# Kernel tuning notes

Measured on AMD Instinct MI355X. Metric: run time of the kernel, lower is better.

Reference implementation:

```python
import jax, jax.numpy as jnp
import numpy as np

B, T, V = 8, 2048, 4096
BEAM = 8      # beam_size
BLANK = 0     # blank_id=0 in CTCBeamDecoder
TMP = 1.0     # temperature self.tmp


def setup_inputs() -> dict:
    key = jax.random.key(0)
    k1, k2 = jax.random.split(key)
    logits = jax.random.normal(k1, (B, T, V), dtype=jnp.float32)
    # valid frame counts in [T//2, T]
    lengths = jax.random.randint(k2, (B,), T // 2, T + 1).astype(jnp.int32)
    return {"logits": logits, "lengths": lengths}


def _beam_search_single(logP, length):
    """CTC beam search over alignments (no LM) for one utterance.
    logP: [T, V] log-probs, length: scalar valid frame count.
    Returns (collapsed_tokens [T] padded with -1, out_len, best_score).
    """
    scores0, toks0 = jax.lax.top_k(logP[0], BEAM)              # [BEAM]
    toks0 = toks0.astype(jnp.int32)
    bp0 = jnp.zeros((BEAM,), jnp.int32)

    def step(scores, xs):
        t, logp_t = xs
        cand = scores[:, None] + logp_t[None, :]               # [BEAM, V]
        new_scores, flat_idx = jax.lax.top_k(cand.reshape(-1), BEAM)
        bp = (flat_idx // V).astype(jnp.int32)
        tok = (flat_idx % V).astype(jnp.int32)
        valid = t < length
        new_scores = jnp.where(valid, new_scores, scores)
        bp = jnp.where(valid, bp, jnp.arange(BEAM, dtype=jnp.int32))
        tok = jnp.where(valid, tok, jnp.full((BEAM,), BLANK, jnp.int32))
        return new_scores, (tok, bp)

    ts = jnp.arange(1, T)
    final_scores, (toks, bps) = jax.lax.scan(step, scores0, (ts, logP[1:]))
    toks = jnp.concatenate([toks0[None], toks], axis=0)        # [T, BEAM]
    bps = jnp.concatenate([bp0[None], bps], axis=0)            # [T, BEAM]

    # backtrace best beam (index 0 after final top_k)
    def back(beam, xs):
        tok_t, bp_t = xs
        return bp_t[beam], tok_t[beam]
    _, path = jax.lax.scan(back, jnp.int32(0), (toks, bps), reverse=True)  # [T] in time order

    # CTC collapse: drop blanks and consecutive repeats, restrict to valid frames
    tpos = jnp.arange(T)
    prev = jnp.concatenate([jnp.array([-1], jnp.int32), path[:-1]])
    keep = (path != BLANK) & (path != prev) & (tpos < length)
    out_len = keep.sum().astype(jnp.int32)
    pos = jnp.cumsum(keep) - 1                                  # target slot for kept tokens
    idx = jnp.where(keep, pos, T)                               # dump non-kept into slot T
    out = jnp.full((T + 1,), -1, jnp.int32).at[idx].set(jnp.where(keep, path, -1))
    return out[:T], out_len, final_scores[0]


def reference(logits, lengths):
    # logits/tmp then log_softmax (the tensorized part of the torch module)
    logP = jax.nn.log_softmax(logits / TMP, axis=-1)            # [B, T, V]
    tokens, out_lens, best_scores = jax.vmap(_beam_search_single)(logP, lengths)
    return tokens, out_lens, best_scores, logP
```

## Files before the change

kernel.cpp:

```cpp
#include <hip/hip_runtime.h>
#include <cmath>

#define NB 8
#define NT 2048
#define NV 4096
#define NK 12

__device__ __forceinline__ void lds_fence() {
  asm volatile("s_waitcnt lgkmcnt(0)" ::: "memory");
}

__global__ __launch_bounds__(64) void lsm_top12_kernel(
    const float* __restrict__ logits,
    float* __restrict__ out_logP,
    float* __restrict__ topPf,
    int* __restrict__ topI)
{
  const int row  = blockIdx.x;
  const int lane = threadIdx.x;
  const float4* __restrict__ x4 = (const float4*)(logits + (size_t)row * NV);

  float m = -INFINITY;
  #pragma unroll 4
  for (int k = 0; k < 16; ++k) {
    float4 f = x4[lane + (k << 6)];
    m = fmaxf(m, fmaxf(fmaxf(f.x, f.y), fmaxf(f.z, f.w)));
  }
  #pragma unroll
  for (int off = 32; off > 0; off >>= 1) m = fmaxf(m, __shfl_xor(m, off, 64));

  float a0 = 0.0f, a1 = 0.0f, a2 = 0.0f, a3 = 0.0f;
  #pragma unroll 4
  for (int k = 0; k < 16; ++k) {
    float4 f = x4[lane + (k << 6)];
    a0 += __expf(f.x - m);
    a1 += __expf(f.y - m);
    a2 += __expf(f.z - m);
    a3 += __expf(f.w - m);
  }
  float accf = (a0 + a1) + (a2 + a3);
  #pragma unroll
  for (int off = 32; off > 0; off >>= 1) accf += __shfl_xor(accf, off, 64);
  const float L32 = logf(accf);

  float lv[NK]; int li[NK];
  #pragma unroll
  for (int z = 0; z < NK; ++z) { lv[z] = -INFINITY; li[z] = 0x7FFFFFFF; }

#define INS(VAL, IDX)                                                       \
  do {                                                                      \
    float _v = (VAL); int _i = (IDX);                                       \
    if (_v > lv[NK - 1]) {                                                  \
      lv[NK - 1] = _v; li[NK - 1] = _i;                                     \
      for (int z = NK - 1; z > 0; --z)                                      \
        if (lv[z] > lv[z - 1]) {                                            \
          float tv = lv[z]; lv[z] = lv[z - 1]; lv[z - 1] = tv;              \
          int   ti = li[z]; li[z] = li[z - 1]; li[z - 1] = ti;              \
        }                                                                   \
    }                                                                       \
  } while (0)

  float4* __restrict__ orow4 = (float4*)(out_logP + (size_t)row * NV);
  #pragma unroll 2
  for (int k = 0; k < 16; ++k) {
    float4 f = x4[lane + (k << 6)];
    int vb = (lane + (k << 6)) << 2;
    float4 o;
    o.x = (f.x - m) - L32;
    o.y = (f.y - m) - L32;
    o.z = (f.z - m) - L32;
    o.w = (f.w - m) - L32;
    orow4[lane + (k << 6)] = o;
    INS(o.x, vb); INS(o.y, vb + 1); INS(o.z, vb + 2); INS(o.w, vb + 3);
  }
#undef INS

  float mv = 0.0f; int mi = 0;
  #pragma unroll
  for (int r = 0; r < NK; ++r) {
    float cv = lv[0]; int ci = li[0];
    #pragma unroll
    for (int off = 32; off > 0; off >>= 1) {
      float ov = __shfl_xor(cv, off, 64);
      int   oi = __shfl_xor(ci, off, 64);
      if (ov > cv || (ov == cv && oi < ci)) { cv = ov; ci = oi; }
    }
    if (r == 0)    { mv = cv; mi = ci; }
    if (lane == r) { mv = cv; mi = ci; }
    if (lv[0] == cv && li[0] == ci) {
      for (int z = 0; z < NK - 1; ++z) { lv[z] = lv[z + 1]; li[z] = li[z + 1]; }
      lv[NK - 1] = -INFINITY; li[NK - 1] = 0x7FFFFFFF;
    }
  }
  if (lane < NK) {
    topPf[(size_t)row * NK + lane] = mv;
    topI [(size_t)row * NK + lane] = mi;
  }
}


#define LOADROW(P, V, R)                                                      \
  do {                                                                        \
    const int _r = (R) < NT ? (R) : (NT - 1);                                 \
    P = Pb[(size_t)_r * NK + j_l];                                            \
    V = Ib[(size_t)_r * NK + j_l];                                            \
  } while (0)

#define STEP(T, PV, VV)                                                       \
  do {                                                                        \
    const float cand = s + (PV);              \
    unsigned int cb = __float_as_uint(cand);                                  \
    cb ^= (unsigned int)((int)cb >> 31) | 0x80000000u;                        \
    const unsigned int flat = (unsigned int)((i_l << 12) | (VV));             \
    const unsigned long long key =                                            \
        ((unsigned long long)cb << 15) | (unsigned long long)(0x7FFFu ^ flat);\
    const unsigned int klo = (unsigned int)key;                               \
    const unsigned int khi = (unsigned int)(key >> 32);                       \
    int rank = 0;                                                             \
    _Pragma("unroll")                                                         \
    for (int mm = 0; mm < 31; ++mm) {                                         \
      const unsigned int olo =                                                \
          (unsigned int)__builtin_amdgcn_readlane((int)klo, mm);              \
      const unsigned int ohi =                                                \
          (unsigned int)__builtin_amdgcn_readlane((int)khi, mm);              \
      const unsigned long long ok = ((unsigned long long)ohi << 32) | olo;    \
      rank += (ok > key) ? 1 : 0;                                             \
    }                                                                         \
      \
    const bool win = active && (rank < 8);                                    \
    const int sloti = win ? ((T) * 8 + rank) : (NT * 8 + lane);               \
    tokbp[sloti] = (unsigned short)(((VV) << 3) | i_l);                       \
    const int dst4 = win ? (rank << 2) : park4;                               \
    const int pushed =                                                        \
        __builtin_amdgcn_ds_permute(dst4, __float_as_int(cand));              \
    const float w0 = __uint_as_float((unsigned)__builtin_amdgcn_readlane(pushed, 0)); \
    const float w1 = __uint_as_float((unsigned)__builtin_amdgcn_readlane(pushed, 1)); \
    const float w2 = __uint_as_float((unsigned)__builtin_amdgcn_readlane(pushed, 2)); \
    const float w3 = __uint_as_float((unsigned)__builtin_amdgcn_readlane(pushed, 3)); \
    const float w4 = __uint_as_float((unsigned)__builtin_amdgcn_readlane(pushed, 4)); \
    const float w5 = __uint_as_float((unsigned)__builtin_amdgcn_readlane(pushed, 5)); \
    const float w6 = __uint_as_float((unsigned)__builtin_amdgcn_readlane(pushed, 6)); \
    const float w7 = __uint_as_float((unsigned)__builtin_amdgcn_readlane(pushed, 7)); \
    const float sA_ = b0 ? w1 : w0;                                           \
    const float sB_ = b0 ? w3 : w2;                                           \
    const float sC_ = b0 ? w5 : w4;                                           \
    const float sD_ = b0 ? w7 : w6;                                           \
    const float sE_ = b1 ? sB_ : sA_;                                         \
    const float sF_ = b1 ? sD_ : sC_;                                         \
    s = b2 ? sF_ : sE_;                                                       \
  } while (0)

__global__ __launch_bounds__(64) void beam_kernel(
    const float* __restrict__ topPf,
    const int* __restrict__ topI,
    const int* __restrict__ lengths,
    float* __restrict__ out_tok,
    float* __restrict__ out_lenA,
    float* __restrict__ out_scr)
{
  const int b    = blockIdx.x;
  const int lane = threadIdx.x;

  __shared__ unsigned short tokbp[NT * 8 + 64];
  __shared__ unsigned short pathA[NT];

  int len = lengths[b];
  if (len < 1) len = 1;
  if (len > NT) len = NT;

  int i_l = 0, j_l = 0; bool active = false;
  {
    int c = 0;
    #pragma unroll
    for (int i = 0; i < 8; ++i) {
      const int cnt = 12 / (i + 1);
      if (lane >= c && lane < c + cnt) { i_l = i; j_l = lane - c; active = true; }
      c += cnt;
    }
  }
  const bool b0 = (i_l & 1) != 0;
  const bool b1 = (i_l & 2) != 0;
  const bool b2 = (i_l & 4) != 0;
  const int  park4 = (32 + (lane & 31)) << 2;

  const float* __restrict__ Pb = topPf + (size_t)b * NT * NK;
  const int*   __restrict__ Ib = topI  + (size_t)b * NT * NK;

  float s = Pb[i_l];
  if (lane < 8) tokbp[lane] = (unsigned short)(Ib[lane] << 3);

  float pA0, pA1, pA2, pA3, pB0, pB1, pB2, pB3;
  int   vA0, vA1, vA2, vA3, vB0, vB1, vB2, vB3;
  LOADROW(pA0, vA0, 1); LOADROW(pA1, vA1, 2);
  LOADROW(pA2, vA2, 3); LOADROW(pA3, vA3, 4);
  LOADROW(pB0, vB0, 5); LOADROW(pB1, vB1, 6);
  LOADROW(pB2, vB2, 7); LOADROW(pB3, vB3, 8);

  int t = 1;
  for (; t + 7 < len; t += 8) {
    STEP(t,     pA0, vA0);
    STEP(t + 1, pA1, vA1);
    STEP(t + 2, pA2, vA2);
    STEP(t + 3, pA3, vA3);
    LOADROW(pA0, vA0, t + 8);  LOADROW(pA1, vA1, t + 9);
    LOADROW(pA2, vA2, t + 10); LOADROW(pA3, vA3, t + 11);
    STEP(t + 4, pB0, vB0);
    STEP(t + 5, pB1, vB1);
    STEP(t + 6, pB2, vB2);
    STEP(t + 7, pB3, vB3);
    LOADROW(pB0, vB0, t + 12); LOADROW(pB1, vB1, t + 13);
    LOADROW(pB2, vB2, t + 14); LOADROW(pB3, vB3, t + 15);
  }
  if (t     < len) STEP(t,     pA0, vA0);
  if (t + 1 < len) STEP(t + 1, pA1, vA1);
  if (t + 2 < len) STEP(t + 2, pA2, vA2);
  if (t + 3 < len) STEP(t + 3, pA3, vA3);
  if (t + 4 < len) STEP(t + 4, pB0, vB0);
  if (t + 5 < len) STEP(t + 5, pB1, vB1);
  if (t + 6 < len) STEP(t + 6, pB2, vB2);

  lds_fence();
  if (lane == 0) {
    const uint4* __restrict__ rows = (const uint4*)tokbp;
#define EXT(R)                                                                \
    do {                                                                      \
      const unsigned long long half = (beam < 4)                              \
          ? (((unsigned long long)(R).y << 32) | (R).x)                       \
          : (((unsigned long long)(R).w << 32) | (R).z);                      \
      const int e = (int)((half >> ((beam & 3) << 4)) & 0xFFFFu);             \
      pathA[bt] = (unsigned short)(e >> 3);                                   \
      beam = e & 7;                                                           \
      --bt;                                                                   \
    } while (0)
    int beam = 0;
    int bt = len - 1;
    uint4 r0 = rows[bt];
    uint4 r1 = rows[bt >= 1 ? bt - 1 : 0];
    uint4 r2 = rows[bt >= 2 ? bt - 2 : 0];
    uint4 r3 = rows[bt >= 3 ? bt - 3 : 0];
    while (bt >= 7) {
      const uint4 n0 = rows[bt - 4], n1 = rows[bt - 5];
      const uint4 n2 = rows[bt - 6], n3 = rows[bt - 7];
      EXT(r0); EXT(r1); EXT(r2); EXT(r3);
      r0 = n0; r1 = n1; r2 = n2; r3 = n3;
    }
    while (bt >= 0) { const uint4 rr = rows[bt]; EXT(rr); }
#undef EXT
  }
  lds_fence();

  const int CH = NT / 64;
  const int base = lane * CH;
  int cnt = 0;
  for (int k = 0; k < CH; ++k) {
    int tt = base + k;
    if (tt < len) {
      int pt = pathA[tt];
      int pv = (tt > 0) ? (int)pathA[tt - 1] : -1;
      cnt += ((pt != 0) && (pt != pv)) ? 1 : 0;
    }
  }
  int incl = cnt;
  #pragma unroll
  for (int off = 1; off < 64; off <<= 1) {
    int n = __shfl_up(incl, off, 64);
    if (lane >= off) incl += n;
  }
  const int excl  = incl - cnt;
  const int total = __shfl(incl, 63, 64);

  float* __restrict__ ob = out_tok + (size_t)b * NT;
  int pos = excl;
  for (int k = 0; k < CH; ++k) {
    int tt = base + k;
    if (tt < len) {
      int pt = pathA[tt];
      int pv = (tt > 0) ? (int)pathA[tt - 1] : -1;
      if ((pt != 0) && (pt != pv)) { ob[pos] = (float)pt; ++pos; }
    }
  }
  for (int q = total + lane; q < NT; q += 64) ob[q] = -1.0f;

  if (lane == 0) {
    out_lenA[b] = (float)total;
    out_scr[b]  = s;
  }
}

#undef STEP
#undef LOADROW

extern "C" void kernel_launch(void* const* d_in, const int* in_sizes, int n_in,
                              void* d_out, int out_size, void* d_ws, size_t ws_size,
                              hipStream_t stream) {
  (void)in_sizes; (void)n_in; (void)out_size; (void)ws_size;
  const float* logits  = (const float*)d_in[0];
  const int*   lengths = (const int*)d_in[1];

  float* out_tok  = (float*)d_out;
  float* out_lenp = out_tok + NB * NT;
  float* out_scr  = out_lenp + NB;
  float* out_logP = out_scr + NB;

  float* topPf = (float*)d_ws;
  int*   topI  = (int*)(topPf + (size_t)NB * NT * NK);

  lsm_top12_kernel<<<NB * NT, 64, 0, stream>>>(logits, out_logP, topPf, topI);
  beam_kernel<<<NB, 64, 0, stream>>>(topPf, topI, lengths, out_tok, out_lenp, out_scr);
}
```

Before: 1.374 ms.

## Cache logits row in registers, gate top-k inserts, prefetch beam inputs into cache

The log-softmax/top-12 kernel now loads each row once into a 16-entry float4 register array instead of reading global memory three times. It also skips the per-element insertion sort when the max of a float4 group cannot enter the list, and sets an occupancy hint in the launch bounds. The beam kernel simplifies the sortable-key transform to a bitwise NOT, valid because candidate scores are always negative. It also adds a warm-up pass that streams the whole per-batch top-k table so later dependent loads hit in cache. The cost is higher register pressure and an extra read of the table.

```diff
diff --git a/kernel.cpp b/kernel.cpp
--- a/kernel.cpp
+++ b/kernel.cpp
@@ -10,7 +10,7 @@
   asm volatile("s_waitcnt lgkmcnt(0)" ::: "memory");
 }
 
-__global__ __launch_bounds__(64) void lsm_top12_kernel(
+__global__ __launch_bounds__(64, 4) void lsm_top12_kernel(
     const float* __restrict__ logits,
     float* __restrict__ out_logP,
     float* __restrict__ topPf,
@@ -20,23 +20,24 @@
   const int lane = threadIdx.x;
   const float4* __restrict__ x4 = (const float4*)(logits + (size_t)row * NV);
 
+  float4 r[16];
+  #pragma unroll
+  for (int k = 0; k < 16; ++k) r[k] = x4[lane + (k << 6)];
+
   float m = -INFINITY;
-  #pragma unroll 4
+  #pragma unroll
+  for (int k = 0; k < 16; ++k)
+    m = fmaxf(m, fmaxf(fmaxf(r[k].x, r[k].y), fmaxf(r[k].z, r[k].w)));
+  #pragma unroll
+  for (int off = 32; off > 0; off >>= 1) m = fmaxf(m, __shfl_xor(m, off, 64));
+
+  float a0 = 0.0f, a1 = 0.0f, a2 = 0.0f, a3 = 0.0f;
+  #pragma unroll
   for (int k = 0; k < 16; ++k) {
-    float4 f = x4[lane + (k << 6)];
-    m = fmaxf(m, fmaxf(fmaxf(f.x, f.y), fmaxf(f.z, f.w)));
-  }
-  #pragma unroll
-  for (int off = 32; off > 0; off >>= 1) m = fmaxf(m, __shfl_xor(m, off, 64));
-
-  float a0 = 0.0f, a1 = 0.0f, a2 = 0.0f, a3 = 0.0f;
-  #pragma unroll 4
-  for (int k = 0; k < 16; ++k) {
-    float4 f = x4[lane + (k << 6)];
-    a0 += __expf(f.x - m);
-    a1 += __expf(f.y - m);
-    a2 += __expf(f.z - m);
-    a3 += __expf(f.w - m);
+    a0 += __expf(r[k].x - m);
+    a1 += __expf(r[k].y - m);
+    a2 += __expf(r[k].z - m);
+    a3 += __expf(r[k].w - m);
   }
   float accf = (a0 + a1) + (a2 + a3);
   #pragma unroll
@@ -61,23 +62,25 @@
   } while (0)
 
   float4* __restrict__ orow4 = (float4*)(out_logP + (size_t)row * NV);
-  #pragma unroll 2
+  #pragma unroll
   for (int k = 0; k < 16; ++k) {
-    float4 f = x4[lane + (k << 6)];
-    int vb = (lane + (k << 6)) << 2;
+    const int vb = (lane + (k << 6)) << 2;
     float4 o;
-    o.x = (f.x - m) - L32;
-    o.y = (f.y - m) - L32;
-    o.z = (f.z - m) - L32;
-    o.w = (f.w - m) - L32;
+    o.x = (r[k].x - m) - L32;
+    o.y = (r[k].y - m) - L32;
+    o.z = (r[k].z - m) - L32;
+    o.w = (r[k].w - m) - L32;
     orow4[lane + (k << 6)] = o;
-    INS(o.x, vb); INS(o.y, vb + 1); INS(o.z, vb + 2); INS(o.w, vb + 3);
+    const float g4 = fmaxf(fmaxf(o.x, o.y), fmaxf(o.z, o.w));
+    if (g4 > lv[NK - 1]) {
+      INS(o.x, vb); INS(o.y, vb + 1); INS(o.z, vb + 2); INS(o.w, vb + 3);
+    }
   }
 #undef INS
 
   float mv = 0.0f; int mi = 0;
   #pragma unroll
-  for (int r = 0; r < NK; ++r) {
+  for (int rr = 0; rr < NK; ++rr) {
     float cv = lv[0]; int ci = li[0];
     #pragma unroll
     for (int off = 32; off > 0; off >>= 1) {
@@ -85,8 +88,8 @@
       int   oi = __shfl_xor(ci, off, 64);
       if (ov > cv || (ov == cv && oi < ci)) { cv = ov; ci = oi; }
     }
-    if (r == 0)    { mv = cv; mi = ci; }
-    if (lane == r) { mv = cv; mi = ci; }
+    if (rr == 0)    { mv = cv; mi = ci; }
+    if (lane == rr) { mv = cv; mi = ci; }
     if (lv[0] == cv && li[0] == ci) {
       for (int z = 0; z < NK - 1; ++z) { lv[z] = lv[z + 1]; li[z] = li[z + 1]; }
       lv[NK - 1] = -INFINITY; li[NK - 1] = 0x7FFFFFFF;
@@ -109,8 +112,7 @@
 #define STEP(T, PV, VV)                                                       \
   do {                                                                        \
     const float cand = s + (PV);              \
-    unsigned int cb = __float_as_uint(cand);                                  \
-    cb ^= (unsigned int)((int)cb >> 31) | 0x80000000u;                        \
+    const unsigned int cb = ~__float_as_uint(cand);                           \
     const unsigned int flat = (unsigned int)((i_l << 12) | (VV));             \
     const unsigned long long key =                                            \
         ((unsigned long long)cb << 15) | (unsigned long long)(0x7FFFu ^ flat);\
@@ -126,7 +128,6 @@
       const unsigned long long ok = ((unsigned long long)ohi << 32) | olo;    \
       rank += (ok > key) ? 1 : 0;                                             \
     }                                                                         \
-      \
     const bool win = active && (rank < 8);                                    \
     const int sloti = win ? ((T) * 8 + rank) : (NT * 8 + lane);               \
     tokbp[sloti] = (unsigned short)(((VV) << 3) | i_l);                       \
@@ -185,6 +186,19 @@
 
   const float* __restrict__ Pb = topPf + (size_t)b * NT * NK;
   const int*   __restrict__ Ib = topI  + (size_t)b * NT * NK;
+
+  {
+    const float4* __restrict__ gp = (const float4*)Pb;
+    const int4*   __restrict__ gi = (const int4*)Ib;
+    float fa = 0.0f; int ia = 0;
+    #pragma unroll 4
+    for (int q = lane; q < NT * NK / 4; q += 64) {
+      const float4 v = gp[q]; const int4 w = gi[q];
+      fa += (v.x + v.y) + (v.z + v.w);
+      ia ^= (w.x ^ w.y) ^ (w.z ^ w.w);
+    }
+    asm volatile("" :: "v"(fa), "v"(ia));
+  }
 
   float s = Pb[i_l];
   if (lane < 8) tokbp[lane] = (unsigned short)(Ib[lane] << 3);
```

Measured after the change: 1.334 ms. -2.9%, faster.
